# Performance work log

Measured on AMD Instinct MI355X. Metric: run time of the kernel, lower is better.

## Reference

```python
import jax, jax.numpy as jnp
import numpy as np

NUM_HEADS = 48
EMBED_DIM = 768


def setup_inputs() -> dict:
    key = jax.random.key(0)
    ks = jax.random.split(key, 12)
    b, n, e, n_exp = 2, 512, EMBED_DIM, 256
    m = n + n_exp  # expanded kv length (periodic images appended)
    s = 0.02
    return {
        "query": jax.random.normal(ks[0], (b, n, e), jnp.float32),
        "attn_bias": jax.random.normal(ks[1], (b * NUM_HEADS, n, m), jnp.float32),
        "delta_pos": jax.random.normal(ks[2], (b, n, m, 3), jnp.float32),
        "outcell_index": jax.random.randint(ks[3], (b, n_exp), 0, n, jnp.int32),
        "Wq": jax.random.normal(ks[4], (e, e), jnp.float32) * s,
        "bq": jnp.zeros((e,), jnp.float32),
        "Wk": jax.random.normal(ks[5], (e, e), jnp.float32) * s,
        "bk": jnp.zeros((e,), jnp.float32),
        "Wv": jax.random.normal(ks[6], (e, e), jnp.float32) * s,
        "bv": jnp.zeros((e,), jnp.float32),
        "w_force": jax.random.normal(ks[7], (e,), jnp.float32) * s,
    }


def reference(query, attn_bias, delta_pos, outcell_index, Wq, bq, Wk, bk, Wv, bv, w_force):
    b, n, e = query.shape
    H = NUM_HEADS
    d = e // H
    scaling = d ** (-0.5)

    def proj(W, bias):
        # [b, n, e] -> [b, H, n, d]
        return (query @ W.T + bias).reshape(b, n, H, d).transpose(0, 2, 1, 3)

    q = proj(Wq, bq) * scaling
    k = proj(Wk, bk)
    v = proj(Wv, bv)

    # periodic-image KV expansion: gather nodes along axis 2, concat
    idx = outcell_index[:, None, :, None]  # [b, 1, n_exp, 1] broadcasts over H, d
    k = jnp.concatenate([k, jnp.take_along_axis(k, idx, axis=2)], axis=2)
    v = jnp.concatenate([v, jnp.take_along_axis(v, idx, axis=2)], axis=2)
    m = k.shape[2]  # n_node_expand

    attn = jnp.einsum('bhnd,bhmd->bhnm', q, k)
    probs = jax.nn.softmax(attn + attn_bias.reshape(b, H, n, m), axis=-1)
    # dropout p=0.1 is identity in eval mode

    # position-weighted value aggregation: [b,h,n,m]*[b,n,m,3] contracted with v over m
    x = jnp.einsum('bhnm,bnmc,bhmd->bnchd', probs, delta_pos, v).reshape(b, n, 3, e)
    force = jnp.einsum('bnce,e->bnc', x, w_force).astype(jnp.float32)  # [b, n, 3]
    return force
```

## Files before the change

kernel.cpp:

```cpp
#include <hip/hip_runtime.h>
#include <cstdint>
#include <cstddef>

#define BDIM 2
#define NQ 512
#define NEXP 256
#define MDIM 768
#define HN 48
#define DD 16
#define ED 768

typedef short v8s __attribute__((ext_vector_type(8)));
typedef float v4f __attribute__((ext_vector_type(4)));

__global__ void prep_kernel(const float* __restrict__ Wv, const float* __restrict__ bv,
                            const float* __restrict__ wf,
                            float* __restrict__ wve, float* __restrict__ ube) {
  int h = blockIdx.x;
  float wl[DD];
#pragma unroll
  for (int d = 0; d < DD; ++d) wl[d] = wf[h * DD + d];
  for (int k = threadIdx.x; k < ED; k += blockDim.x) {
    float s = 0.f;
#pragma unroll
    for (int d = 0; d < DD; ++d) s = fmaf(wl[d], Wv[(size_t)(h * DD + d) * ED + k], s);
    wve[(size_t)h * ED + k] = s;
  }
  if (threadIdx.x == 0) {
    float s = 0.f;
#pragma unroll
    for (int d = 0; d < DD; ++d) s = fmaf(wl[d], bv[h * DD + d], s);
    ube[h] = s;
  }
}

__global__ __launch_bounds__(256) void convert_kernel(
    const float* __restrict__ query, const float* __restrict__ Wq,
    const float* __restrict__ Wk, const float* __restrict__ wve,
    ushort* __restrict__ Abf, ushort* __restrict__ Bbf) {
  const int id = blockIdx.x * 256 + threadIdx.x;
  const float* src = nullptr;
  ushort* dst;
  if (id < 98304) {
    const int off = id * 8;
    src = query + off;
    dst = Abf + off;
  } else {
    const int id2 = id - 98304;
    const int r = id2 / 96;
    const int k = (id2 - r * 96) * 8;
    dst = Bbf + (size_t)r * 768 + k;
    if (r < 768)       src = Wq + (size_t)r * 768 + k;
    else if (r < 1536) src = Wk + (size_t)(r - 768) * 768 + k;
    else if (r < 1584) src = wve + (size_t)(r - 1536) * 768 + k;
  }
  union { ushort s[8]; uint4 v; } p;
  if (src) {
    const float4 v0 = *(const float4*)src;
    const float4 v1 = *(const float4*)(src + 4);
    const float vv[8] = {v0.x, v0.y, v0.z, v0.w, v1.x, v1.y, v1.z, v1.w};
#pragma unroll
    for (int i = 0; i < 8; ++i) {
      union { float f; uint32_t u; } c; c.f = vv[i];
      p.s[i] = (ushort)((c.u + 0x7FFFu + ((c.u >> 16) & 1u)) >> 16);
    }
  } else {
#pragma unroll
    for (int i = 0; i < 8; ++i) p.s[i] = 0;
  }
  *(uint4*)dst = p.v;
}

__global__ __launch_bounds__(256) void proj_mfma(
    const ushort* __restrict__ Abf, const ushort* __restrict__ Bbf,
    const float* __restrict__ bq, const float* __restrict__ bk,
    const float* __restrict__ ube,
    float* __restrict__ qs, float* __restrict__ ke, float* __restrict__ ub) {
  __shared__ __align__(16) ushort As[4][4][16][8];
  __shared__ __align__(16) ushort Bs[4][64][8];
  const int tid = threadIdx.x;
  const int wave = tid >> 6, lane = tid & 63;
  const int m0 = blockIdx.y * 64, n0 = blockIdx.x * 64;
  const int arow = tid >> 2;
  const int aseg = tid & 3;
  v4f acc[4] = {v4f{0,0,0,0}, v4f{0,0,0,0}, v4f{0,0,0,0}, v4f{0,0,0,0}};

  for (int k0 = 0; k0 < ED; k0 += 32) {
    __syncthreads();
    *(uint4*)&As[arow >> 4][aseg][arow & 15][0] =
        *(const uint4*)&Abf[(size_t)(m0 + arow) * ED + k0 + aseg * 8];
    *(uint4*)&Bs[aseg][arow][0] =
        *(const uint4*)&Bbf[(size_t)(n0 + arow) * ED + k0 + aseg * 8];
    __syncthreads();
    const v8s af = *(const v8s*)&As[wave][lane >> 4][lane & 15][0];
#pragma unroll
    for (int nt = 0; nt < 4; ++nt) {
      const v8s bfr = *(const v8s*)&Bs[lane >> 4][nt * 16 + (lane & 15)][0];
      acc[nt] = __builtin_amdgcn_mfma_f32_16x16x32_bf16(af, bfr, acc[nt], 0, 0, 0);
    }
  }

#pragma unroll
  for (int nt = 0; nt < 4; ++nt) {
    const int c = n0 + nt * 16 + (lane & 15);
    if (c >= 1584) continue;
#pragma unroll
    for (int r = 0; r < 4; ++r) {
      const int row = m0 + wave * 16 + (lane >> 4) * 4 + r;
      const int b = row >> 9, n = row & 511;
      const float val = acc[nt][r];
      if (c < 768) {
        qs[(size_t)(b * NQ + n) * ED + c] = (val + bq[c]) * 0.25f;
      } else if (c < 1536) {
        const int ck = c - 768;
        const int hh = ck >> 4, dd = ck & 15;
        ke[(size_t)((b * HN + hh) * DD + dd) * MDIM + n] = val + bk[ck];
      } else {
        const int hh = c - 1536;
        ub[(size_t)(b * HN + hh) * MDIM + n] = val + ube[hh];
      }
    }
  }
}

__global__ void gather_kernel(const int* __restrict__ idx, float* __restrict__ ke,
                              float* __restrict__ ub) {
  const int id = blockIdx.x * 256 + threadIdx.x;
  const int N1 = BDIM * HN * DD * NEXP;
  if (id < N1) {
    int j = id & (NEXP - 1);
    int d = (id >> 8) & (DD - 1);
    int hb = id >> 12;
    int n = idx[(hb / HN) * NEXP + j];
    float* row = ke + (size_t)(hb * DD + d) * MDIM;
    row[NQ + j] = row[n];
  } else {
    int id2 = id - N1;
    if (id2 < BDIM * HN * NEXP) {
      int j = id2 & (NEXP - 1);
      int hb = id2 >> 8;
      int n = idx[(hb / HN) * NEXP + j];
      float* row = ub + (size_t)hb * MDIM;
      row[NQ + j] = row[n];
    }
  }
}

__device__ __forceinline__ void fma4(float4& a, float q, const float4& k) {
  a.x = fmaf(q, k.x, a.x); a.y = fmaf(q, k.y, a.y);
  a.z = fmaf(q, k.z, a.z); a.w = fmaf(q, k.w, a.w);
}

__global__ __launch_bounds__(256) void fused_kernel(
    const float* __restrict__ qs, const float* __restrict__ ke, const float* __restrict__ ub,
    const float* __restrict__ bias, float* __restrict__ Wp) {
  __shared__ __align__(16) float Wl[2][4 * MDIM];
  const int bid = blockIdx.x;
  const int b = bid & 1;
  const int hg = (bid >> 1) & 3;
  const int n0 = (bid >> 3) * 4;
  const int wave = threadIdx.x >> 6;
  const int lane = threadIdx.x & 63;
  const int hbase = hg * 12 + wave * 3;

  float4 wacc[4][3] = {};
  float4 a[4][3];

#pragma unroll
  for (int qi = 0; qi < 4; ++qi) {
    const float4* bp = (const float4*)(bias + (size_t)((b * HN + hbase) * NQ + n0 + qi) * MDIM);
#pragma unroll
    for (int j = 0; j < 3; ++j) a[qi][j] = bp[lane + 64 * j];
  }

  for (int hi = 0; hi < 3; ++hi) {
    const int h = hbase + hi;
    const float* kbase = ke + (size_t)(b * HN + h) * DD * MDIM;
    const float4* u4 = (const float4*)(ub + (size_t)(b * HN + h) * MDIM);
    const float4 u0 = u4[lane], u1 = u4[lane + 64], u2 = u4[lane + 128];

#pragma unroll
    for (int x = 0; x < 4; ++x) {
      float4 qx[4];
#pragma unroll
      for (int qi = 0; qi < 4; ++qi)
        qx[qi] = ((const float4*)(qs + (size_t)(b * NQ + n0 + qi) * ED + h * DD))[x];
#pragma unroll
      for (int d4 = 0; d4 < 4; ++d4) {
        const float4* kr = (const float4*)(kbase + (size_t)(x * 4 + d4) * MDIM);
        const float4 k0 = kr[lane], k1 = kr[lane + 64], k2 = kr[lane + 128];
#pragma unroll
        for (int qi = 0; qi < 4; ++qi) {
          const float qd = (d4 == 0) ? qx[qi].x : (d4 == 1) ? qx[qi].y
                          : (d4 == 2) ? qx[qi].z : qx[qi].w;
          fma4(a[qi][0], qd, k0);
          fma4(a[qi][1], qd, k1);
          fma4(a[qi][2], qd, k2);
        }
      }
    }
#pragma unroll
    for (int qi = 0; qi < 4; ++qi) {
      float mx = -1e30f;
#pragma unroll
      for (int j = 0; j < 3; ++j)
        mx = fmaxf(mx, fmaxf(fmaxf(a[qi][j].x, a[qi][j].y), fmaxf(a[qi][j].z, a[qi][j].w)));
#pragma unroll
      for (int sh = 32; sh > 0; sh >>= 1) mx = fmaxf(mx, __shfl_xor(mx, sh));
      float e[12];
#pragma unroll
      for (int j = 0; j < 3; ++j) {
        e[j * 4 + 0] = __expf(a[qi][j].x - mx);
        e[j * 4 + 1] = __expf(a[qi][j].y - mx);
        e[j * 4 + 2] = __expf(a[qi][j].z - mx);
        e[j * 4 + 3] = __expf(a[qi][j].w - mx);
      }
      if (hi < 2) {
        const float4* bp = (const float4*)(bias + (size_t)((b * HN + h + 1) * NQ + n0 + qi) * MDIM);
#pragma unroll
        for (int j = 0; j < 3; ++j) a[qi][j] = bp[lane + 64 * j];
      }
      float l = 0.f;
#pragma unroll
      for (int k = 0; k < 12; ++k) l += e[k];
#pragma unroll
      for (int sh = 32; sh > 0; sh >>= 1) l += __shfl_xor(l, sh);
      const float inv = 1.0f / l;
#pragma unroll
      for (int j = 0; j < 3; ++j) {
        const float4 uu = (j == 0) ? u0 : (j == 1) ? u1 : u2;
        wacc[qi][j].x = fmaf(e[j * 4 + 0] * inv, uu.x, wacc[qi][j].x);
        wacc[qi][j].y = fmaf(e[j * 4 + 1] * inv, uu.y, wacc[qi][j].y);
        wacc[qi][j].z = fmaf(e[j * 4 + 2] * inv, uu.z, wacc[qi][j].z);
        wacc[qi][j].w = fmaf(e[j * 4 + 3] * inv, uu.w, wacc[qi][j].w);
      }
    }
  }

  if (wave >= 2) {
    float4* dst = (float4*)Wl[wave - 2];
#pragma unroll
    for (int qi = 0; qi < 4; ++qi)
#pragma unroll
      for (int j = 0; j < 3; ++j) dst[qi * 192 + lane + 64 * j] = wacc[qi][j];
  }
  __syncthreads();
  if (wave < 2) {
    float4* dst = (float4*)Wl[wave];
#pragma unroll
    for (int qi = 0; qi < 4; ++qi)
#pragma unroll
      for (int j = 0; j < 3; ++j) {
        float4 t = dst[qi * 192 + lane + 64 * j];
        t.x += wacc[qi][j].x; t.y += wacc[qi][j].y;
        t.z += wacc[qi][j].z; t.w += wacc[qi][j].w;
        dst[qi * 192 + lane + 64 * j] = t;
      }
  }
  __syncthreads();

  const float4* w0 = (const float4*)Wl[0];
  const float4* w1 = (const float4*)Wl[1];
  float4* wp = (float4*)Wp;
  for (int f = threadIdx.x; f < 768; f += 256) {
    const int qi = f / 192, mf = f % 192;
    float4 s = w0[f];
    const float4 t = w1[f];
    s.x += t.x; s.y += t.y; s.z += t.z; s.w += t.w;
    wp[((size_t)(b * NQ + n0 + qi) * 4 + hg) * 192 + mf] = s;
  }
}

__global__ __launch_bounds__(256) void force_kernel(
    const float* __restrict__ Wp, const float* __restrict__ dp, float* __restrict__ out) {
  const int wave = threadIdx.x >> 6;
  const int lane = threadIdx.x & 63;
  const int row = blockIdx.x * 4 + wave;
  const float4* wp = (const float4*)Wp;
  float4 ws[3];
#pragma unroll
  for (int j = 0; j < 3; ++j) {
    float4 s = wp[((size_t)row * 4 + 0) * 192 + lane + 64 * j];
#pragma unroll
    for (int hg = 1; hg < 4; ++hg) {
      const float4 t = wp[((size_t)row * 4 + hg) * 192 + lane + 64 * j];
      s.x += t.x; s.y += t.y; s.z += t.z; s.w += t.w;
    }
    ws[j] = s;
  }
  const float* dpp = dp + (size_t)row * MDIM * 3;
  float f0 = 0.f, f1 = 0.f, f2 = 0.f;
#pragma unroll
  for (int j = 0; j < 3; ++j) {
    const float4 w = ws[j];
    const int m0 = j * 256 + lane * 4;
    const float4* dv = (const float4*)(dpp + (size_t)m0 * 3);
    const float4 d0 = dv[0], d1 = dv[1], d2 = dv[2];
    f0 = fmaf(w.x, d0.x, f0); f0 = fmaf(w.y, d0.w, f0); f0 = fmaf(w.z, d1.z, f0); f0 = fmaf(w.w, d2.y, f0);
    f1 = fmaf(w.x, d0.y, f1); f1 = fmaf(w.y, d1.x, f1); f1 = fmaf(w.z, d1.w, f1); f1 = fmaf(w.w, d2.z, f1);
    f2 = fmaf(w.x, d0.z, f2); f2 = fmaf(w.y, d1.y, f2); f2 = fmaf(w.z, d2.x, f2); f2 = fmaf(w.w, d2.w, f2);
  }
#pragma unroll
  for (int sh = 32; sh > 0; sh >>= 1) {
    f0 += __shfl_xor(f0, sh);
    f1 += __shfl_xor(f1, sh);
    f2 += __shfl_xor(f2, sh);
  }
  if (lane == 0) {
    float* op = out + (size_t)row * 3;
    op[0] = f0; op[1] = f1; op[2] = f2;
  }
}

extern "C" void kernel_launch(void* const* d_in, const int* in_sizes, int n_in,
                              void* d_out, int out_size, void* d_ws, size_t ws_size,
                              hipStream_t stream) {
  const float* query     = (const float*)d_in[0];
  const float* attn_bias = (const float*)d_in[1];
  const float* delta_pos = (const float*)d_in[2];
  const int*   outcell   = (const int*)d_in[3];
  const float* Wq = (const float*)d_in[4];
  const float* bq = (const float*)d_in[5];
  const float* Wk = (const float*)d_in[6];
  const float* bk = (const float*)d_in[7];
  const float* Wv = (const float*)d_in[8];
  const float* bv = (const float*)d_in[9];
  const float* wf = (const float*)d_in[10];
  float* out = (float*)d_out;
  float* ws  = (float*)d_ws;

  float* wve  = ws;
  float* ube  = ws + 36864;
  float* qsb  = ws + 36928;
  float* keb  = ws + 823360;
  float* ubb  = ws + 2003008;
  float* Wpb  = ws + 2076736;
  ushort* Abf = (ushort*)(ws + 5222464);
  ushort* Bbf = (ushort*)(ws + 5615680);

  prep_kernel<<<HN, 256, 0, stream>>>(Wv, bv, wf, wve, ube);
  convert_kernel<<<984, 256, 0, stream>>>(query, Wq, Wk, wve, Abf, Bbf);
  proj_mfma<<<dim3(25, 16), 256, 0, stream>>>(Abf, Bbf, bq, bk, ube, qsb, keb, ubb);
  gather_kernel<<<1632, 256, 0, stream>>>(outcell, keb, ubb);
  fused_kernel<<<1024, 256, 0, stream>>>(qsb, keb, ubb, attn_bias, Wpb);
  force_kernel<<<256, 256, 0, stream>>>(Wpb, delta_pos, out);
}
```

Measured before the change: 314.3 us.

## Split fused kernel waves over query pairs and six heads, cut registers

Each wave now handles 2 query rows across 6 heads instead of 4 query rows across 3 heads. This halves the per-wave accumulator and score register arrays, and launch bounds now request 4 blocks per CU for higher occupancy. The cross-wave reduction shrinks to a single LDS pass with one barrier, and global writes go straight from registers. In exchange, each K row load is reused across only 2 queries instead of 4, which doubles K/U traffic per query.

```diff
diff --git a/kernel.cpp b/kernel.cpp
--- a/kernel.cpp
+++ b/kernel.cpp
@@ -151,29 +151,32 @@
   a.z = fmaf(q, k.z, a.z); a.w = fmaf(q, k.w, a.w);
 }
 
-__global__ __launch_bounds__(256) void fused_kernel(
+__global__ __launch_bounds__(256, 4) void fused_kernel(
     const float* __restrict__ qs, const float* __restrict__ ke, const float* __restrict__ ub,
     const float* __restrict__ bias, float* __restrict__ Wp) {
-  __shared__ __align__(16) float Wl[2][4 * MDIM];
+  __shared__ __align__(16) float Wl[2][2][3][64 * 4];
   const int bid = blockIdx.x;
   const int b = bid & 1;
   const int hg = (bid >> 1) & 3;
   const int n0 = (bid >> 3) * 4;
   const int wave = threadIdx.x >> 6;
   const int lane = threadIdx.x & 63;
-  const int hbase = hg * 12 + wave * 3;
-
-  float4 wacc[4][3] = {};
-  float4 a[4][3];
-
-#pragma unroll
-  for (int qi = 0; qi < 4; ++qi) {
-    const float4* bp = (const float4*)(bias + (size_t)((b * HN + hbase) * NQ + n0 + qi) * MDIM);
+  const int qp = wave >> 1;
+  const int hh = wave & 1;
+  const int hbase = hg * 12 + hh * 6;
+  const int r0 = n0 + qp * 2;
+
+  float4 wacc[2][3] = {};
+  float4 a[2][3];
+
+#pragma unroll
+  for (int qi = 0; qi < 2; ++qi) {
+    const float4* bp = (const float4*)(bias + (size_t)((b * HN + hbase) * NQ + r0 + qi) * MDIM);
 #pragma unroll
     for (int j = 0; j < 3; ++j) a[qi][j] = bp[lane + 64 * j];
   }
 
-  for (int hi = 0; hi < 3; ++hi) {
+  for (int hi = 0; hi < 6; ++hi) {
     const int h = hbase + hi;
     const float* kbase = ke + (size_t)(b * HN + h) * DD * MDIM;
     const float4* u4 = (const float4*)(ub + (size_t)(b * HN + h) * MDIM);
@@ -181,16 +184,16 @@
 
 #pragma unroll
     for (int x = 0; x < 4; ++x) {
-      float4 qx[4];
-#pragma unroll
-      for (int qi = 0; qi < 4; ++qi)
-        qx[qi] = ((const float4*)(qs + (size_t)(b * NQ + n0 + qi) * ED + h * DD))[x];
+      float4 qx[2];
+#pragma unroll
+      for (int qi = 0; qi < 2; ++qi)
+        qx[qi] = ((const float4*)(qs + (size_t)(b * NQ + r0 + qi) * ED + h * DD))[x];
 #pragma unroll
       for (int d4 = 0; d4 < 4; ++d4) {
         const float4* kr = (const float4*)(kbase + (size_t)(x * 4 + d4) * MDIM);
         const float4 k0 = kr[lane], k1 = kr[lane + 64], k2 = kr[lane + 128];
 #pragma unroll
-        for (int qi = 0; qi < 4; ++qi) {
+        for (int qi = 0; qi < 2; ++qi) {
           const float qd = (d4 == 0) ? qx[qi].x : (d4 == 1) ? qx[qi].y
                           : (d4 == 2) ? qx[qi].z : qx[qi].w;
           fma4(a[qi][0], qd, k0);
@@ -200,7 +203,7 @@
       }
     }
 #pragma unroll
-    for (int qi = 0; qi < 4; ++qi) {
+    for (int qi = 0; qi < 2; ++qi) {
       float mx = -1e30f;
 #pragma unroll
       for (int j = 0; j < 3; ++j)
@@ -215,8 +218,8 @@
         e[j * 4 + 2] = __expf(a[qi][j].z - mx);
         e[j * 4 + 3] = __expf(a[qi][j].w - mx);
       }
-      if (hi < 2) {
-        const float4* bp = (const float4*)(bias + (size_t)((b * HN + h + 1) * NQ + n0 + qi) * MDIM);
+      if (hi < 5) {
+        const float4* bp = (const float4*)(bias + (size_t)((b * HN + h + 1) * NQ + r0 + qi) * MDIM);
 #pragma unroll
         for (int j = 0; j < 3; ++j) a[qi][j] = bp[lane + 64 * j];
       }
@@ -237,37 +240,26 @@
     }
   }
 
-  if (wave >= 2) {
-    float4* dst = (float4*)Wl[wave - 2];
-#pragma unroll
-    for (int qi = 0; qi < 4; ++qi)
-#pragma unroll
-      for (int j = 0; j < 3; ++j) dst[qi * 192 + lane + 64 * j] = wacc[qi][j];
+  if (hh == 1) {
+    float4* dst = (float4*)&Wl[qp][0][0][0];
+#pragma unroll
+    for (int qi = 0; qi < 2; ++qi)
+#pragma unroll
+      for (int j = 0; j < 3; ++j) dst[(qi * 3 + j) * 64 + lane] = wacc[qi][j];
   }
   __syncthreads();
-  if (wave < 2) {
-    float4* dst = (float4*)Wl[wave];
-#pragma unroll
-    for (int qi = 0; qi < 4; ++qi)
+  if (hh == 0) {
+    const float4* src = (const float4*)&Wl[qp][0][0][0];
+    float4* wp = (float4*)Wp;
+#pragma unroll
+    for (int qi = 0; qi < 2; ++qi)
 #pragma unroll
       for (int j = 0; j < 3; ++j) {
-        float4 t = dst[qi * 192 + lane + 64 * j];
+        float4 t = src[(qi * 3 + j) * 64 + lane];
         t.x += wacc[qi][j].x; t.y += wacc[qi][j].y;
         t.z += wacc[qi][j].z; t.w += wacc[qi][j].w;
-        dst[qi * 192 + lane + 64 * j] = t;
-      }
-  }
-  __syncthreads();
-
-  const float4* w0 = (const float4*)Wl[0];
-  const float4* w1 = (const float4*)Wl[1];
-  float4* wp = (float4*)Wp;
-  for (int f = threadIdx.x; f < 768; f += 256) {
-    const int qi = f / 192, mf = f % 192;
-    float4 s = w0[f];
-    const float4 t = w1[f];
-    s.x += t.x; s.y += t.y; s.z += t.z; s.w += t.w;
-    wp[((size_t)(b * NQ + n0 + qi) * 4 + hg) * 192 + mf] = s;
+        wp[((size_t)(b * NQ + r0 + qi) * 4 + hg) * 192 + lane + 64 * j] = t;
+      }
   }
 }
 
```

Result: slower. 1.018 ms (+224.0%).
